# Kernel tuning notes

Hardware: AMD Instinct MI355X
Metric: run time of the kernel (lower is better)

Reference implementation:

```python
import jax, jax.numpy as jnp
import numpy as np

N = 4096
D_IN = 1024
D_OUT = 512
DENSITY = 0.005
LRELU_ALPHA = 0.2  # tf.nn.leaky_relu default


def _make_adj(key):
    # sparse binary adjacency, symmetric, with self-loops (dense 0/1 float mask)
    a = (jax.random.uniform(key, (N, N)) < DENSITY).astype(jnp.float32)
    a = jnp.maximum(a, a.T)
    a = jnp.maximum(a, jnp.eye(N, dtype=jnp.float32))
    return a


def setup_inputs() -> dict:
    key = jax.random.key(0)
    ks = jax.random.split(key, 7)
    x = jax.random.normal(ks[0], (N, D_IN), dtype=jnp.float32)
    adj = _make_adj(ks[1])
    # glorot-ish scales
    Wf = jax.random.normal(ks[2], (D_IN, D_OUT), dtype=jnp.float32) * (1.0 / np.sqrt(D_IN))
    a1 = jax.random.normal(ks[3], (D_OUT, 1), dtype=jnp.float32) * (1.0 / np.sqrt(D_OUT))
    b1 = jnp.zeros((1,), dtype=jnp.float32)
    a2 = jax.random.normal(ks[4], (D_OUT, 1), dtype=jnp.float32) * (1.0 / np.sqrt(D_OUT))
    b2 = jnp.zeros((1,), dtype=jnp.float32)
    W = jax.random.normal(ks[5], (D_IN, D_OUT), dtype=jnp.float32) * (1.0 / np.sqrt(D_IN))
    return {"x": x, "adj": adj, "Wf": Wf, "a1": a1, "b1": b1, "a2": a2, "b2": b2, "W": W}


def reference(x, adj, Wf, a1, b1, a2, b2, W):
    # dropout = 0 (inference) -> identity; coef dropout skipped for determinism
    mask = adj != 0.0
    # conv1d(kernel=1) == pointwise linear
    seq_fts = x @ Wf                      # [N, D_OUT]
    f1 = seq_fts @ a1 + b1                # [N, 1]
    f2 = seq_fts @ a2 + b2                # [N, 1]
    # sparse logits: adj_ij * f1_i + adj_ij * f2_j on edges
    logits = adj * f1 + adj * f2.T        # [N, N]
    lrelu = jnp.where(logits >= 0, logits, LRELU_ALPHA * logits)
    # sparse softmax over edge entries per row
    masked = jnp.where(mask, lrelu, -jnp.inf)
    coefs = jax.nn.softmax(masked, axis=1)
    coefs = jnp.where(mask, coefs, 0.0)
    # symmetrize: (coefs + coefs^T)/2
    coefs = (coefs + coefs.T) * 0.5
    # coefs_I = diag(rowsum^0) = I  (pow(x,0)==1)
    coefs_mat = coefs + jnp.eye(N, dtype=coefs.dtype)
    rowsum = jnp.sum(coefs_mat, axis=1, keepdims=True)   # [N,1], >= 1
    d_inv_sqrt = rowsum ** -0.5
    d_inv_inverse = d_inv_sqrt ** -1.0
    inf_int = jnp.isinf(d_inv_sqrt).astype(jnp.float32)
    d = (d_inv_inverse + inf_int) ** -1.0 - inf_int
    d = jnp.sum(d, axis=1)                # [N]
    d_mat = jnp.diag(d)                   # [N,N] diagonal matrix
    # NOTE: original uses ELEMENTWISE multiply with the diag matrix (faithful):
    support_mat = (coefs_mat * d_mat).T * d_mat   # effectively diagonal
    pre_sup = x @ W                       # [N, D_OUT]
    out = support_mat @ pre_sup           # [N, D_OUT]
    return jax.nn.relu(out)
```

## Files before the change

kernel.cpp:

```cpp
#include <hip/hip_runtime.h>
#include <stdint.h>
#include <math.h>

#define NN 4096
#define DIN 1024
#define DOUT 512
#define ALPHA 0.2f

typedef __attribute__((ext_vector_type(8))) short short8;
typedef __attribute__((ext_vector_type(4))) float f32x4;

__device__ __forceinline__ unsigned short f2bf(float f) {
    uint32_t u = __float_as_uint(f);
    u += 0x7fffu + ((u >> 16) & 1u);
    return (unsigned short)(u >> 16);
}

__device__ __forceinline__ void async16(const void* g, void* l) {
    __builtin_amdgcn_global_load_lds(
        (const __attribute__((address_space(1))) uint32_t*)g,
        (__attribute__((address_space(3))) uint32_t*)l, 16, 0, 0);
}

__global__ __launch_bounds__(256) void k_prep(const float* __restrict__ W,
                                              const float* __restrict__ Wf,
                                              const float* __restrict__ a1,
                                              const float* __restrict__ a2,
                                              unsigned short* __restrict__ wt,
                                              float* __restrict__ wa1,
                                              float* __restrict__ wa2) {
    int tid = threadIdx.x;
    if (blockIdx.x < 256) {
        int bx = blockIdx.x & 7, gy = blockIdx.x >> 3;
        int n = bx * 64 + (tid & 63);
        int g = gy * 4 + (tid >> 6);
        float v[8];
#pragma unroll
        for (int j = 0; j < 8; ++j) v[j] = W[(size_t)(g * 8 + j) * DOUT + n];
        union { unsigned short u[8]; uint4 q; } pk;
#pragma unroll
        for (int j = 0; j < 8; ++j) pk.u[j] = f2bf(v[j]);
        int sw = (n >> 1) & 3;
        int p  = (g & ~3) | ((g & 3) ^ sw);
        *(uint4*)(wt + (size_t)n * DIN + p * 8) = pk.q;
    } else {
        int row  = (blockIdx.x - 256) * 4 + (tid >> 6);
        int lane = tid & 63;
        const float* wr = Wf + (size_t)row * DOUT;
        float s1 = 0.f, s2 = 0.f;
        for (int k = lane; k < DOUT; k += 64) {
            float w = wr[k];
            s1 += w * a1[k];
            s2 += w * a2[k];
        }
        for (int off = 32; off; off >>= 1) {
            s1 += __shfl_down(s1, off);
            s2 += __shfl_down(s2, off);
        }
        if (lane == 0) { wa1[row] = s1; wa2[row] = s2; }
    }
}

__global__ __launch_bounds__(256) void k_maskfx(const float* __restrict__ adj,
    const float* __restrict__ x,
    const float* __restrict__ wa1, const float* __restrict__ wa2,
    const float* __restrict__ b1, const float* __restrict__ b2,
    float* __restrict__ f1, float* __restrict__ f2,
    unsigned short* __restrict__ xb,
    unsigned short* __restrict__ bits16) {
    int tid = threadIdx.x;
    if (blockIdx.x < 2048) {
        int row0 = blockIdx.x * 2;
        const float4* a0 = (const float4*)(adj + (size_t)row0 * NN);
        const float4* a1v = (const float4*)(adj + (size_t)(row0 + 1) * NN);
        float4 v0 = a0[tid];        float4 v1 = a0[tid + 256];
        float4 v2 = a0[tid + 512];  float4 v3 = a0[tid + 768];
        float4 v4 = a1v[tid];       float4 v5 = a1v[tid + 256];
        float4 v6 = a1v[tid + 512]; float4 v7 = a1v[tid + 768];
        __builtin_amdgcn_sched_barrier(0);
        unsigned int m0 = 0, m1 = 0;
#define MB(M, V, J)                                            \
        M |= (((V).x != 0.f) ? 1u : 0u) << (4 * (J));          \
        M |= (((V).y != 0.f) ? 1u : 0u) << (4 * (J) + 1);      \
        M |= (((V).z != 0.f) ? 1u : 0u) << (4 * (J) + 2);      \
        M |= (((V).w != 0.f) ? 1u : 0u) << (4 * (J) + 3);
        MB(m0, v0, 0) MB(m0, v1, 1) MB(m0, v2, 2) MB(m0, v3, 3)
        MB(m1, v4, 0) MB(m1, v5, 1) MB(m1, v6, 2) MB(m1, v7, 3)
#undef MB
        bits16[(size_t)row0 * 256 + tid]       = (unsigned short)m0;
        bits16[(size_t)row0 * 256 + 256 + tid] = (unsigned short)m1;
    } else {
        int row  = (blockIdx.x - 2048) * 4 + (tid >> 6);
        int lane = tid & 63;
        const float* xr = x + (size_t)row * DIN + lane * 16;
        float xv[16];
        *(float4*)&xv[0]  = *(const float4*)(xr);
        *(float4*)&xv[4]  = *(const float4*)(xr + 4);
        *(float4*)&xv[8]  = *(const float4*)(xr + 8);
        *(float4*)&xv[12] = *(const float4*)(xr + 12);
        __builtin_amdgcn_sched_barrier(0);
        const float* w1 = wa1 + lane * 16;
        const float* w2 = wa2 + lane * 16;
        float s1 = 0.f, s2 = 0.f;
#pragma unroll
        for (int j = 0; j < 16; ++j) {
            s1 += xv[j] * w1[j];
            s2 += xv[j] * w2[j];
        }
        union { unsigned short u[8]; uint4 q; } pk0, pk1;
#pragma unroll
        for (int j = 0; j < 8; ++j) { pk0.u[j] = f2bf(xv[j]); pk1.u[j] = f2bf(xv[8 + j]); }
        int sw = (row >> 1) & 3;
        int g0 = lane * 2, g1 = lane * 2 + 1;
        int p0 = (g0 & ~3) | ((g0 & 3) ^ sw);
        int p1 = (g1 & ~3) | ((g1 & 3) ^ sw);
        unsigned short* xrow = xb + (size_t)row * DIN;
        *(uint4*)(xrow + p0 * 8) = pk0.q;
        *(uint4*)(xrow + p1 * 8) = pk1.q;
        for (int off = 32; off; off >>= 1) {
            s1 += __shfl_down(s1, off);
            s2 += __shfl_down(s2, off);
        }
        if (lane == 0) { f1[row] = s1 + b1[0]; f2[row] = s2 + b2[0]; }
    }
}

__global__ __launch_bounds__(256) void k_z(const unsigned long long* __restrict__ bits,
                                           const float* __restrict__ f1,
                                           const float* __restrict__ f2,
                                           float* __restrict__ rZ_out) {
    int row  = blockIdx.x * 4 + (threadIdx.x >> 6);
    int lane = threadIdx.x & 63;
    unsigned long long w = bits[(size_t)row * 64 + lane];
    float f1r = f1[row];
    float z = 0.f;
    while (w) {
        int b = __builtin_ctzll(w);
        w &= w - 1;
        int j = 16 * lane + 4 * (b >> 4) + 1024 * ((b >> 2) & 3) + (b & 3);
        float l = f1r + f2[j];
        z += __expf((l >= 0.f) ? l : ALPHA * l);
    }
    for (int off = 32; off; off >>= 1) z += __shfl_down(z, off);
    if (lane == 0) rZ_out[row] = 1.0f / z;
}

__global__ __launch_bounds__(256) void k_s(const unsigned long long* __restrict__ bits,
                                           const float* __restrict__ f1,
                                           const float* __restrict__ f2,
                                           const float* __restrict__ rZ,
                                           float* __restrict__ s_out) {
    int row  = blockIdx.x * 4 + (threadIdx.x >> 6);
    int lane = threadIdx.x & 63;
    unsigned long long w = bits[(size_t)row * 64 + lane];
    float f2r = f2[row];
    float sum = 0.f;
    while (w) {
        int b = __builtin_ctzll(w);
        w &= w - 1;
        int j = 16 * lane + 4 * (b >> 4) + 1024 * ((b >> 2) & 3) + (b & 3);
        float l = f1[j] + f2r;
        float e = (l >= 0.f) ? l : ALPHA * l;
        sum += __expf(e) * rZ[j];
    }
    for (int off = 32; off; off >>= 1) sum += __shfl_down(sum, off);
    if (lane == 0) {
        float l   = f1[row] + f2r;
        float e   = (l >= 0.f) ? l : ALPHA * l;
        float cjj = __expf(e) * rZ[row];
        s_out[row] = (cjj + 1.0f) / (1.5f + 0.5f * sum);
    }
}

__global__ __launch_bounds__(256) void k_gemm(const unsigned short* __restrict__ xb,
                                              const unsigned short* __restrict__ wt,
                                              const float* __restrict__ s,
                                              float* __restrict__ out) {
    __shared__ __align__(16) unsigned short As[2][64][32];
    __shared__ __align__(16) unsigned short Bs[2][64][32];
    int lid = blockIdx.y * gridDim.x + blockIdx.x;
    int xcd = lid & 7, idx = lid >> 3;
    int by = xcd * 8 + (idx & 7);
    int bx = idx >> 3;
    int bm = by * 64, bn = bx * 64;

    int tid = threadIdx.x, wid = tid >> 6, lane = tid & 63;
    int wr = wid >> 1, wc = wid & 1;

    int srow = lane >> 2, sg = lane & 3;
    const unsigned short* ga0 = xb + (size_t)(bm + wid * 16 + srow) * DIN + sg * 8;
    const unsigned short* gb0 = wt + (size_t)(bn + wid * 16 + srow) * DIN + sg * 8;

    int r15 = lane & 15, gl = lane >> 4;
    int gofs = (gl ^ ((r15 >> 1) & 3)) * 8;

    f32x4 acc[2][2] = {};

#define STAGE(BUF, K0) do {                                              \
        async16(ga0 + (K0), &As[BUF][wid * 16][0]);                      \
        async16(gb0 + (K0), &Bs[BUF][wid * 16][0]);                      \
    } while (0)

#define COMPUTE(BUF) do {                                                \
        const unsigned short* pa = &As[BUF][wr * 32 + r15][gofs];        \
        const unsigned short* pb = &Bs[BUF][wc * 32 + r15][gofs];        \
        short8 af0 = *(const short8*)(pa);                               \
        short8 af1 = *(const short8*)(pa + 16 * 32);                     \
        short8 bf0 = *(const short8*)(pb);                               \
        short8 bf1 = *(const short8*)(pb + 16 * 32);                     \
        acc[0][0] = __builtin_amdgcn_mfma_f32_16x16x32_bf16(af0, bf0, acc[0][0], 0, 0, 0); \
        acc[0][1] = __builtin_amdgcn_mfma_f32_16x16x32_bf16(af0, bf1, acc[0][1], 0, 0, 0); \
        acc[1][0] = __builtin_amdgcn_mfma_f32_16x16x32_bf16(af1, bf0, acc[1][0], 0, 0, 0); \
        acc[1][1] = __builtin_amdgcn_mfma_f32_16x16x32_bf16(af1, bf1, acc[1][1], 0, 0, 0); \
    } while (0)

    STAGE(0, 0);
    asm volatile("s_waitcnt vmcnt(0)" ::: "memory");
    __syncthreads();
    int cur = 0;
    for (int t = 0; t < (DIN / 32) - 1; ++t) {
        STAGE(cur ^ 1, (t + 1) * 32);
        COMPUTE(cur);
        asm volatile("s_waitcnt vmcnt(0)" ::: "memory");
        __syncthreads();
        cur ^= 1;
    }
    COMPUTE(cur);

#pragma unroll
    for (int mi = 0; mi < 2; ++mi) {
        int crow0 = bm + wr * 32 + mi * 16 + gl * 4;
#pragma unroll
        for (int ni = 0; ni < 2; ++ni) {
            int ccol = bn + wc * 32 + ni * 16 + r15;
#pragma unroll
            for (int r = 0; r < 4; ++r) {
                int row = crow0 + r;
                float v = acc[mi][ni][r] * s[row];
                out[(size_t)row * DOUT + ccol] = fmaxf(v, 0.f);
            }
        }
    }
#undef STAGE
#undef COMPUTE
}

extern "C" void kernel_launch(void* const* d_in, const int* in_sizes, int n_in,
                              void* d_out, int out_size, void* d_ws, size_t ws_size,
                              hipStream_t stream) {
    const float* x   = (const float*)d_in[0];
    const float* adj = (const float*)d_in[1];
    const float* Wf  = (const float*)d_in[2];
    const float* a1  = (const float*)d_in[3];
    const float* b1  = (const float*)d_in[4];
    const float* a2  = (const float*)d_in[5];
    const float* b2  = (const float*)d_in[6];
    const float* W   = (const float*)d_in[7];
    float* out = (float*)d_out;

    char* w = (char*)d_ws;
    float* wa1 = (float*)(w + 0);
    float* wa2 = (float*)(w + 4096);
    float* f1  = (float*)(w + 16384);
    float* f2  = (float*)(w + 32768);
    float* rZ  = (float*)(w + 49152);
    float* s   = (float*)(w + 65536);
    unsigned short* bits16 = (unsigned short*)(w + 98304);
    unsigned short* xb = (unsigned short*)(w + 2195456);
    unsigned short* wt = (unsigned short*)(w + 10584064);

    k_prep<<<512, 256, 0, stream>>>(W, Wf, a1, a2, wt, wa1, wa2);
    k_maskfx<<<3072, 256, 0, stream>>>(adj, x, wa1, wa2, b1, b2, f1, f2, xb, bits16);
    k_z<<<1024, 256, 0, stream>>>((const unsigned long long*)bits16, f1, f2, rZ);
    k_s<<<1024, 256, 0, stream>>>((const unsigned long long*)bits16, f1, f2, rZ, s);
    dim3 gg(8, 64);
    k_gemm<<<gg, 256, 0, stream>>>(xb, wt, s, out);
}
```

Before: 49.38 us.

## Triple-buffer GEMM k-loop and fold W transpose into mask kernel

The GEMM k-loop now uses three LDS buffers with a partial vmcnt wait, so global loads for two stages ahead stay in flight while the current tile is computed. The W bf16 transpose/pack moves from the prep kernel into the mask/x-conversion kernel as extra blocks, leaving a lighter prep kernel that only computes Wf·a. The aim is to hide load latency in the GEMM and shorten the serial prep stage, at the cost of more LDS use per block.

```diff
diff --git a/kernel.cpp b/kernel.cpp
--- a/kernel.cpp
+++ b/kernel.cpp
@@ -22,51 +22,33 @@
         (__attribute__((address_space(3))) uint32_t*)l, 16, 0, 0);
 }
 
-__global__ __launch_bounds__(256) void k_prep(const float* __restrict__ W,
-                                              const float* __restrict__ Wf,
-                                              const float* __restrict__ a1,
-                                              const float* __restrict__ a2,
-                                              unsigned short* __restrict__ wt,
-                                              float* __restrict__ wa1,
-                                              float* __restrict__ wa2) {
-    int tid = threadIdx.x;
-    if (blockIdx.x < 256) {
-        int bx = blockIdx.x & 7, gy = blockIdx.x >> 3;
-        int n = bx * 64 + (tid & 63);
-        int g = gy * 4 + (tid >> 6);
-        float v[8];
-#pragma unroll
-        for (int j = 0; j < 8; ++j) v[j] = W[(size_t)(g * 8 + j) * DOUT + n];
-        union { unsigned short u[8]; uint4 q; } pk;
-#pragma unroll
-        for (int j = 0; j < 8; ++j) pk.u[j] = f2bf(v[j]);
-        int sw = (n >> 1) & 3;
-        int p  = (g & ~3) | ((g & 3) ^ sw);
-        *(uint4*)(wt + (size_t)n * DIN + p * 8) = pk.q;
-    } else {
-        int row  = (blockIdx.x - 256) * 4 + (tid >> 6);
-        int lane = tid & 63;
-        const float* wr = Wf + (size_t)row * DOUT;
-        float s1 = 0.f, s2 = 0.f;
-        for (int k = lane; k < DOUT; k += 64) {
-            float w = wr[k];
-            s1 += w * a1[k];
-            s2 += w * a2[k];
-        }
-        for (int off = 32; off; off >>= 1) {
-            s1 += __shfl_down(s1, off);
-            s2 += __shfl_down(s2, off);
-        }
-        if (lane == 0) { wa1[row] = s1; wa2[row] = s2; }
-    }
+__global__ __launch_bounds__(256) void k_wa(const float* __restrict__ Wf,
+                                            const float* __restrict__ a1,
+                                            const float* __restrict__ a2,
+                                            float* __restrict__ wa1,
+                                            float* __restrict__ wa2) {
+    int row  = blockIdx.x * 4 + (threadIdx.x >> 6);
+    int lane = threadIdx.x & 63;
+    const float* wr = Wf + (size_t)row * DOUT;
+    float s1 = 0.f, s2 = 0.f;
+    for (int k = lane; k < DOUT; k += 64) {
+        float w = wr[k];
+        s1 += w * a1[k];
+        s2 += w * a2[k];
+    }
+    for (int off = 32; off; off >>= 1) {
+        s1 += __shfl_down(s1, off);
+        s2 += __shfl_down(s2, off);
+    }
+    if (lane == 0) { wa1[row] = s1; wa2[row] = s2; }
 }
 
 __global__ __launch_bounds__(256) void k_maskfx(const float* __restrict__ adj,
-    const float* __restrict__ x,
+    const float* __restrict__ x, const float* __restrict__ W,
     const float* __restrict__ wa1, const float* __restrict__ wa2,
     const float* __restrict__ b1, const float* __restrict__ b2,
     float* __restrict__ f1, float* __restrict__ f2,
-    unsigned short* __restrict__ xb,
+    unsigned short* __restrict__ xb, unsigned short* __restrict__ wt,
     unsigned short* __restrict__ bits16) {
     int tid = threadIdx.x;
     if (blockIdx.x < 2048) {
@@ -89,7 +71,7 @@
 #undef MB
         bits16[(size_t)row0 * 256 + tid]       = (unsigned short)m0;
         bits16[(size_t)row0 * 256 + 256 + tid] = (unsigned short)m1;
-    } else {
+    } else if (blockIdx.x < 3072) {
         int row  = (blockIdx.x - 2048) * 4 + (tid >> 6);
         int lane = tid & 63;
         const float* xr = x + (size_t)row * DIN + lane * 16;
@@ -122,6 +104,20 @@
             s2 += __shfl_down(s2, off);
         }
         if (lane == 0) { f1[row] = s1 + b1[0]; f2[row] = s2 + b2[0]; }
+    } else {
+        int idx = blockIdx.x - 3072;
+        int bx = idx & 7, gy = idx >> 3;
+        int n = bx * 64 + (tid & 63);
+        int g = gy * 4 + (tid >> 6);
+        float v[8];
+#pragma unroll
+        for (int j = 0; j < 8; ++j) v[j] = W[(size_t)(g * 8 + j) * DOUT + n];
+        union { unsigned short u[8]; uint4 q; } pk;
+#pragma unroll
+        for (int j = 0; j < 8; ++j) pk.u[j] = f2bf(v[j]);
+        int sw = (n >> 1) & 3;
+        int p  = (g & ~3) | ((g & 3) ^ sw);
+        *(uint4*)(wt + (size_t)n * DIN + p * 8) = pk.q;
     }
 }
 
@@ -176,8 +172,8 @@
                                               const unsigned short* __restrict__ wt,
                                               const float* __restrict__ s,
                                               float* __restrict__ out) {
-    __shared__ __align__(16) unsigned short As[2][64][32];
-    __shared__ __align__(16) unsigned short Bs[2][64][32];
+    __shared__ __align__(16) unsigned short As[3][64][32];
+    __shared__ __align__(16) unsigned short Bs[3][64][32];
     int lid = blockIdx.y * gridDim.x + blockIdx.x;
     int xcd = lid & 7, idx = lid >> 3;
     int by = xcd * 8 + (idx & 7);
@@ -214,18 +210,24 @@
         acc[1][1] = __builtin_amdgcn_mfma_f32_16x16x32_bf16(af1, bf1, acc[1][1], 0, 0, 0); \
     } while (0)
 
+#define WAITBAR(N) do {                                                  \
+        asm volatile("s_waitcnt vmcnt(" #N ")" ::: "memory");            \
+        __builtin_amdgcn_sched_barrier(0);                               \
+        __builtin_amdgcn_s_barrier();                                    \
+        __builtin_amdgcn_sched_barrier(0);                               \
+    } while (0)
+
     STAGE(0, 0);
-    asm volatile("s_waitcnt vmcnt(0)" ::: "memory");
-    __syncthreads();
-    int cur = 0;
-    for (int t = 0; t < (DIN / 32) - 1; ++t) {
-        STAGE(cur ^ 1, (t + 1) * 32);
-        COMPUTE(cur);
-        asm volatile("s_waitcnt vmcnt(0)" ::: "memory");
-        __syncthreads();
-        cur ^= 1;
-    }
-    COMPUTE(cur);
+    STAGE(1, 32);
+    for (int t = 0; t < 30; ++t) {
+        WAITBAR(2);
+        COMPUTE(t % 3);
+        STAGE((t + 2) % 3, (t + 2) * 32);
+    }
+    WAITBAR(2);
+    COMPUTE(0);
+    WAITBAR(0);
+    COMPUTE(1);
 
 #pragma unroll
     for (int mi = 0; mi < 2; ++mi) {
@@ -243,6 +245,7 @@
     }
 #undef STAGE
 #undef COMPUTE
+#undef WAITBAR
 }
 
 extern "C" void kernel_launch(void* const* d_in, const int* in_sizes, int n_in,
@@ -269,8 +272,9 @@
     unsigned short* xb = (unsigned short*)(w + 2195456);
     unsigned short* wt = (unsigned short*)(w + 10584064);
 
-    k_prep<<<512, 256, 0, stream>>>(W, Wf, a1, a2, wt, wa1, wa2);
-    k_maskfx<<<3072, 256, 0, stream>>>(adj, x, wa1, wa2, b1, b2, f1, f2, xb, bits16);
+    k_wa<<<256, 256, 0, stream>>>(Wf, a1, a2, wa1, wa2);
+    k_maskfx<<<3328, 256, 0, stream>>>(adj, x, W, wa1, wa2, b1, b2,
+                                       f1, f2, xb, wt, bits16);
     k_z<<<1024, 256, 0, stream>>>((const unsigned long long*)bits16, f1, f2, rZ);
     k_s<<<1024, 256, 0, stream>>>((const unsigned long long*)bits16, f1, f2, rZ, s);
     dim3 gg(8, 64);
```

Measured after the change: 43.75 us. 1.13x faster.
